# Kernel tuning notes

Hardware: AMD Instinct MI355X
Metric: run time of the kernel (lower is better)

The kernel has to match this reference:

```python
import jax, jax.numpy as jnp
import numpy as np

N_SEGMENTS = 256  # matches init_kwargs n_segments


def setup_inputs() -> dict:
    key = jax.random.key(0)
    k1, k2 = jax.random.split(key)
    B, H, W, C = 8, 512, 512, 32
    image = jax.random.normal(k1, (B, H, W, C), dtype=jnp.float32)
    # SLIC labels are 1-indexed in the original module (it computes slic - 1 first)
    slic = jax.random.randint(k2, (B, H, W, 1), 1, N_SEGMENTS + 1, dtype=jnp.int32)
    return {"image": image, "slic": slic}


def reference(image, slic):
    # Original: for each segment id s in [1, n_segments], mask pixels where slic == s,
    # segment_avg[c] = sum(image*mask)[c] / count_nonzero(image*mask)[c].
    # NOTE: denominator counts NONZERO masked values per channel (tf.count_nonzero on
    # image*mask), not the raw pixel count of the segment. We replicate that exactly,
    # but in a single O(H*W) segment-sum pass instead of the O(n_segments*H*W) loop.
    B, H, W, C = image.shape
    seg = slic.reshape(B, H * W) - 1            # [B, P] zero-indexed segment ids
    img = image.reshape(B, H * W, C)            # [B, P, C]

    def per_image(x, s):
        sums = jax.ops.segment_sum(x, s, num_segments=N_SEGMENTS)                      # [S, C]
        cnts = jax.ops.segment_sum((x != 0).astype(jnp.float32), s,
                                   num_segments=N_SEGMENTS)                            # [S, C]
        return sums / cnts

    return jax.vmap(per_image)(img, seg)        # [B, N_SEGMENTS, C]
```

## Files before the change

kernel.cpp:

```cpp
#include <hip/hip_runtime.h>


#define HW_PIX (512 * 512)
#define NSEG 256
#define NCH 32
#define BPI 96
#define NBLK (8 * BPI)

__global__ __launch_bounds__(256, 3) void seg_avg_main(
    const float* __restrict__ img, const int* __restrict__ slic,
    float* __restrict__ gsum, unsigned* __restrict__ gcnt)
{
    __shared__ float    s_sum[NSEG][33];
    __shared__ unsigned s_cnt[NSEG][17];

    const int tid = threadIdx.x;
    for (int i = tid; i < NSEG * 33; i += 256) (&s_sum[0][0])[i] = 0.0f;
    for (int i = tid; i < NSEG * 17; i += 256) (&s_cnt[0][0])[i] = 0u;
    __syncthreads();

    const int b   = blockIdx.x / BPI;
    const int blk = blockIdx.x % BPI;
    const int sub = tid & 7;
    const int pl  = tid >> 3;
    const int c0  = sub * 4;

    const float4* __restrict__ imgb =
        (const float4*)(img + (size_t)b * HW_PIX * NCH);
    const int* __restrict__ slicb = slic + (size_t)b * HW_PIX;

    for (int p = blk * 32 + pl; p < HW_PIX; p += BPI * 32) {
        const int seg = slicb[p] - 1;
        const float4 v = imgb[(size_t)p * 8 + sub];

        unsafeAtomicAdd(&s_sum[seg][c0 + 0], v.x);
        unsafeAtomicAdd(&s_sum[seg][c0 + 1], v.y);
        unsafeAtomicAdd(&s_sum[seg][c0 + 2], v.z);
        unsafeAtomicAdd(&s_sum[seg][c0 + 3], v.w);

        const unsigned pk0 = (v.x != 0.0f ? 1u : 0u) | ((v.y != 0.0f ? 1u : 0u) << 16);
        const unsigned pk1 = (v.z != 0.0f ? 1u : 0u) | ((v.w != 0.0f ? 1u : 0u) << 16);
        atomicAdd(&s_cnt[seg][sub * 2 + 0], pk0);
        atomicAdd(&s_cnt[seg][sub * 2 + 1], pk1);
    }
    __syncthreads();

    float*    gs = gsum + (size_t)b * NSEG * NCH;
    unsigned* gc = gcnt + (size_t)b * NSEG * (NCH / 2);
    for (int i = tid; i < NSEG * NCH; i += 256) {
        unsafeAtomicAdd(&gs[i], s_sum[i >> 5][i & 31]);
    }
    for (int i = tid; i < NSEG * (NCH / 2); i += 256) {
        atomicAdd(&gc[i], s_cnt[i >> 4][i & 15]);
    }
}

__global__ __launch_bounds__(256) void seg_avg_final(
    const float* __restrict__ gsum, const unsigned* __restrict__ gcnt,
    float* __restrict__ out)
{
    const int i = blockIdx.x * 256 + threadIdx.x;
    const int c  = i & 31;
    const int bs = i >> 5;
    const unsigned packed = gcnt[bs * 16 + (c >> 1)];
    const float cnt = (float)((packed >> ((c & 1) * 16)) & 0xFFFFu);
    out[i] = gsum[i] / cnt;
}

extern "C" void kernel_launch(void* const* d_in, const int* in_sizes, int n_in,
                              void* d_out, int out_size, void* d_ws, size_t ws_size,
                              hipStream_t stream)
{
    const float* img  = (const float*)d_in[0];
    const int*   slic = (const int*)d_in[1];
    float*       out  = (float*)d_out;

    float*    gsum = (float*)d_ws;
    unsigned* gcnt = (unsigned*)((char*)d_ws + 8 * NSEG * NCH * 4);

    hipMemsetAsync(d_ws, 0, (size_t)(8 * NSEG * NCH * 4 + 8 * NSEG * (NCH / 2) * 4), stream);

    seg_avg_main<<<NBLK, 256, 0, stream>>>(img, slic, gsum, gcnt);
    seg_avg_final<<<(8 * NSEG * NCH) / 256, 256, 0, stream>>>(gsum, gcnt, out);
}
```

Before: 611.6 us.

## Count pixels per segment and subtract rare zeros instead of per-channel nonzero counts

Rather than accumulating per-channel nonzero counts in shared memory, the kernel counts pixels per segment once (one atomic per pixel) and records zero-valued channels through rare global atomics. The final divisor becomes pixel count minus zero count. This removes two LDS atomics per thread per pixel and shrinks shared memory, which allows higher occupancy (launch bounds 4, more blocks per image). It relies on zeros being uncommon; inputs with many zeros would cause heavy global atomic traffic.

```diff
diff --git a/kernel.cpp b/kernel.cpp
--- a/kernel.cpp
+++ b/kernel.cpp
@@ -4,19 +4,20 @@
 #define HW_PIX (512 * 512)
 #define NSEG 256
 #define NCH 32
-#define BPI 96
+#define BPI 128
 #define NBLK (8 * BPI)
 
-__global__ __launch_bounds__(256, 3) void seg_avg_main(
+__global__ __launch_bounds__(256, 4) void seg_avg_main(
     const float* __restrict__ img, const int* __restrict__ slic,
-    float* __restrict__ gsum, unsigned* __restrict__ gcnt)
+    float* __restrict__ gsum, unsigned* __restrict__ gpix,
+    unsigned* __restrict__ gzero)
 {
     __shared__ float    s_sum[NSEG][33];
-    __shared__ unsigned s_cnt[NSEG][17];
+    __shared__ unsigned s_pix[NSEG];
 
     const int tid = threadIdx.x;
     for (int i = tid; i < NSEG * 33; i += 256) (&s_sum[0][0])[i] = 0.0f;
-    for (int i = tid; i < NSEG * 17; i += 256) (&s_cnt[0][0])[i] = 0u;
+    if (tid < NSEG) s_pix[tid] = 0u;
     __syncthreads();
 
     const int b   = blockIdx.x / BPI;
@@ -33,37 +34,38 @@
         const int seg = slicb[p] - 1;
         const float4 v = imgb[(size_t)p * 8 + sub];
 
-        unsafeAtomicAdd(&s_sum[seg][c0 + 0], v.x);
-        unsafeAtomicAdd(&s_sum[seg][c0 + 1], v.y);
-        unsafeAtomicAdd(&s_sum[seg][c0 + 2], v.z);
-        unsafeAtomicAdd(&s_sum[seg][c0 + 3], v.w);
+        atomicAdd(&s_sum[seg][c0 + 0], v.x);
+        atomicAdd(&s_sum[seg][c0 + 1], v.y);
+        atomicAdd(&s_sum[seg][c0 + 2], v.z);
+        atomicAdd(&s_sum[seg][c0 + 3], v.w);
+        if (sub == 0) atomicAdd(&s_pix[seg], 1u);
 
-        const unsigned pk0 = (v.x != 0.0f ? 1u : 0u) | ((v.y != 0.0f ? 1u : 0u) << 16);
-        const unsigned pk1 = (v.z != 0.0f ? 1u : 0u) | ((v.w != 0.0f ? 1u : 0u) << 16);
-        atomicAdd(&s_cnt[seg][sub * 2 + 0], pk0);
-        atomicAdd(&s_cnt[seg][sub * 2 + 1], pk1);
+        const unsigned z = (v.x == 0.0f ? 1u : 0u) | (v.y == 0.0f ? 2u : 0u) |
+                           (v.z == 0.0f ? 4u : 0u) | (v.w == 0.0f ? 8u : 0u);
+        if (z) {
+            unsigned* gz = gzero + ((size_t)(b * NSEG + seg) << 5) + c0;
+            if (z & 1u) atomicAdd(gz + 0, 1u);
+            if (z & 2u) atomicAdd(gz + 1, 1u);
+            if (z & 4u) atomicAdd(gz + 2, 1u);
+            if (z & 8u) atomicAdd(gz + 3, 1u);
+        }
     }
     __syncthreads();
 
     float*    gs = gsum + (size_t)b * NSEG * NCH;
-    unsigned* gc = gcnt + (size_t)b * NSEG * (NCH / 2);
-    for (int i = tid; i < NSEG * NCH; i += 256) {
+    unsigned* gp = gpix + (size_t)b * NSEG;
+    for (int i = tid; i < NSEG * NCH; i += 256)
         unsafeAtomicAdd(&gs[i], s_sum[i >> 5][i & 31]);
-    }
-    for (int i = tid; i < NSEG * (NCH / 2); i += 256) {
-        atomicAdd(&gc[i], s_cnt[i >> 4][i & 15]);
-    }
+    if (tid < NSEG) atomicAdd(&gp[tid], s_pix[tid]);
 }
 
 __global__ __launch_bounds__(256) void seg_avg_final(
-    const float* __restrict__ gsum, const unsigned* __restrict__ gcnt,
-    float* __restrict__ out)
+    const float* __restrict__ gsum, const unsigned* __restrict__ gpix,
+    const unsigned* __restrict__ gzero, float* __restrict__ out)
 {
-    const int i = blockIdx.x * 256 + threadIdx.x;
-    const int c  = i & 31;
+    const int i  = blockIdx.x * 256 + threadIdx.x;
     const int bs = i >> 5;
-    const unsigned packed = gcnt[bs * 16 + (c >> 1)];
-    const float cnt = (float)((packed >> ((c & 1) * 16)) & 0xFFFFu);
+    const float cnt = (float)(gpix[bs] - gzero[i]);
     out[i] = gsum[i] / cnt;
 }
 
@@ -75,11 +77,14 @@
     const int*   slic = (const int*)d_in[1];
     float*       out  = (float*)d_out;
 
-    float*    gsum = (float*)d_ws;
-    unsigned* gcnt = (unsigned*)((char*)d_ws + 8 * NSEG * NCH * 4);
+    float*    gsum  = (float*)d_ws;
+    unsigned* gpix  = (unsigned*)((char*)d_ws + (size_t)8 * NSEG * NCH * 4);
+    unsigned* gzero = (unsigned*)((char*)d_ws + (size_t)8 * NSEG * NCH * 4 + 8 * NSEG * 4);
 
-    hipMemsetAsync(d_ws, 0, (size_t)(8 * NSEG * NCH * 4 + 8 * NSEG * (NCH / 2) * 4), stream);
+    const size_t zero_bytes = (size_t)8 * NSEG * NCH * 4 + 8 * NSEG * 4
+                            + (size_t)8 * NSEG * NCH * 4;
+    hipMemsetAsync(d_ws, 0, zero_bytes, stream);
 
-    seg_avg_main<<<NBLK, 256, 0, stream>>>(img, slic, gsum, gcnt);
-    seg_avg_final<<<(8 * NSEG * NCH) / 256, 256, 0, stream>>>(gsum, gcnt, out);
+    seg_avg_main<<<NBLK, 256, 0, stream>>>(img, slic, gsum, gpix, gzero);
+    seg_avg_final<<<(8 * NSEG * NCH) / 256, 256, 0, stream>>>(gsum, gpix, gzero, out);
 }
```

New measurement: 605.0 us. Within noise of the previous version (-1.1%).
